# Kernel tuning notes

Hardware: AMD Instinct MI355X
Metric: run time of the kernel (lower is better)

The kernel has to match this reference:

```python
import jax, jax.numpy as jnp
import numpy as np

B, S, D, H = 2, 2048, 1024, 16
HEAD_DIM = D // H
SCALE = HEAD_DIM ** -0.5


def setup_inputs() -> dict:
    key = jax.random.key(0)
    k1, k2, k3 = jax.random.split(key, 3)
    x = jax.random.normal(k1, (B, S, D), dtype=jnp.float32)
    # torch nn.Linear convention: weight is [out_features, in_features], y = x @ W.T + b
    W_qkv = jax.random.normal(k2, (3 * D, D), dtype=jnp.float32) * 0.02  # qkv Linear, bias=False
    W_out = jax.random.normal(k3, (D, D), dtype=jnp.float32) * 0.02
    b_out = jnp.zeros((D,), dtype=jnp.float32)
    return {"x": x, "W_qkv": W_qkv, "W_out": W_out, "b_out": b_out}


def reference(x, W_qkv, W_out, b_out):
    b, s, d_model = x.shape
    # qkv projection (no bias), then split 'b c (qkv h d) -> qkv b h c d'
    qkv = (x @ W_qkv.T).reshape(b, s, 3, H, HEAD_DIM).transpose(2, 0, 3, 1, 4)
    q, k, v = qkv[0], qkv[1], qkv[2]  # each [b, h, s, hd]
    # naive full attention: scores materialized as [b, h, s, s]
    attn = jax.nn.softmax(jnp.einsum('bhxd,bhyd->bhxy', q, k) * SCALE, axis=-1)
    # dropout is identity (rate 0 / eval mode)
    o = jnp.einsum('bhxy,bhyd->bhxd', attn, v)
    o = o.transpose(0, 2, 1, 3).reshape(b, s, d_model)  # 'b h c d -> b c (h d)'
    return o @ W_out.T + b_out
```

## Files before the change

### kernel.cpp

```cpp
#include <hip/hip_runtime.h>


typedef __attribute__((ext_vector_type(8))) short short8;
typedef __attribute__((ext_vector_type(4))) float f32x4;
typedef __attribute__((ext_vector_type(2))) unsigned int uint32x2;
typedef unsigned short ushort_t;
typedef unsigned int uint32;

#define AS1 __attribute__((address_space(1)))
#define AS3 __attribute__((address_space(3)))

__device__ __forceinline__ void gload_lds16(const void* gp, void* lp) {
    __builtin_amdgcn_global_load_lds((const AS1 void*)gp, (AS3 void*)lp, 16, 0, 0);
}

#if __has_builtin(__builtin_amdgcn_exp2f)
#define EXP2F(x) __builtin_amdgcn_exp2f(x)
#else
#define EXP2F(x) exp2f(x)
#endif

__device__ __forceinline__ uint32 rhu(float f) { return __float_as_uint(f) + 0x8000u; }
#if __has_builtin(__builtin_amdgcn_perm)
__device__ __forceinline__ uint32 pk2bf(float a, float b) {
    return __builtin_amdgcn_perm(rhu(b), rhu(a), 0x07060302u);
}
#else
__device__ __forceinline__ uint32 pk2bf(float a, float b) {
    return (rhu(a) >> 16) | (rhu(b) & 0xffff0000u);
}
#endif
__device__ __forceinline__ ushort_t f2bf(float f) { return (ushort_t)(rhu(f) >> 16); }

#if __has_builtin(__builtin_amdgcn_permlane32_swap)
__device__ __forceinline__ void plane32(uint32& a, uint32& b) {
    uint32x2 r = __builtin_amdgcn_permlane32_swap(a, b, false, false);
    a = r[0]; b = r[1];
}
#else
__device__ __forceinline__ void plane32(uint32& a, uint32& b) {
    asm("v_permlane32_swap_b32 %0, %1" : "+v"(a), "+v"(b));
}
#endif
#if __has_builtin(__builtin_amdgcn_permlane16_swap)
__device__ __forceinline__ void plane16(uint32& a, uint32& b) {
    uint32x2 r = __builtin_amdgcn_permlane16_swap(a, b, false, false);
    a = r[0]; b = r[1];
}
#else
__device__ __forceinline__ void plane16(uint32& a, uint32& b) {
    asm("v_permlane16_swap_b32 %0, %1" : "+v"(a), "+v"(b));
}
#endif

__global__ void cvt_all(const float* __restrict__ x, ushort_t* __restrict__ xb,
                        const float* __restrict__ wq, ushort_t* __restrict__ wqb,
                        const float* __restrict__ wo, ushort_t* __restrict__ wob) {
    int blk = blockIdx.x;
    const float* in; ushort_t* out;
    if (blk < 4096)      { in = x;  out = xb;  }
    else if (blk < 7168) { in = wq; out = wqb; blk -= 4096; }
    else                 { in = wo; out = wob; blk -= 7168; }
    const int i = (blk * 256 + threadIdx.x) * 4;
    const float4 v = *(const float4*)(in + i);
    uint2 pk;
    pk.x = pk2bf(v.x, v.y);
    pk.y = pk2bf(v.z, v.w);
    *(uint2*)(out + i) = pk;
}

__global__ __launch_bounds__(512, 2)
void gemm_qkv(const ushort_t* __restrict__ A, const ushort_t* __restrict__ B,
              ushort_t* __restrict__ Cb, ushort_t* __restrict__ vT, float qScale) {
    __shared__ ushort_t smem[4][16384];
    const int K = 1024;
    const int tid = threadIdx.x;
    const int wave = tid >> 6, lane = tid & 63;
    const int quad = lane >> 4, l16 = lane & 15;
    const int wr = wave >> 2, wc = wave & 3;

    int bid = blockIdx.x + 12 * blockIdx.y;
    bid = (bid & 7) * 24 + (bid >> 3);
    const int nBase = (bid % 12) * 256, mBase = (bid / 12) * 256;

    f32x4 acc[8][4];
#pragma unroll
    for (int i = 0; i < 8; i++)
#pragma unroll
        for (int j = 0; j < 4; j++) acc[i][j] = (f32x4){0.f, 0.f, 0.f, 0.f};

    const int ar = tid >> 2;
    const int ac = ((tid & 3) ^ ((ar >> 1) & 3)) * 8;
    const int rsw = (l16 >> 1) & 3;

    const ushort_t* aptr = A + (size_t)(mBase + ar) * K + ac;
    const ushort_t* bptr = B + (size_t)(nBase + ar) * K + ac;

#define G1_STAGE(t)                                                                   \
    {                                                                                 \
        ushort_t* d = &smem[(t) & 3][0];                                              \
        const int k0 = (t) * 32;                                                      \
        gload_lds16(aptr + k0, d + wave * 512);                                       \
        gload_lds16(aptr + (size_t)128 * K + k0, d + 4096 + wave * 512);              \
        gload_lds16(bptr + k0, d + 8192 + wave * 512);                                \
        gload_lds16(bptr + (size_t)128 * K + k0, d + 12288 + wave * 512);             \
    }

#define G1_COMPUTE(t)                                                                 \
    {                                                                                 \
        const ushort_t* lA = &smem[(t) & 3][0];                                       \
        const ushort_t* lB = lA + 8192;                                               \
        short8 af[8], bf[4];                                                          \
        _Pragma("unroll") for (int i = 0; i < 8; i++)                                 \
            af[i] = *(const short8*)(lA + (wr * 128 + i * 16 + l16) * 32 +            \
                                     ((quad ^ rsw) * 8));                             \
        _Pragma("unroll") for (int j = 0; j < 4; j++)                                 \
            bf[j] = *(const short8*)(lB + (wc * 64 + j * 16 + l16) * 32 +             \
                                     ((quad ^ rsw) * 8));                             \
        _Pragma("unroll") for (int i = 0; i < 8; i++)                                 \
            _Pragma("unroll") for (int j = 0; j < 4; j++)                             \
                acc[i][j] = __builtin_amdgcn_mfma_f32_16x16x32_bf16(af[i], bf[j],     \
                                                                    acc[i][j], 0, 0, 0); \
    }

#define G1_SYNC(n)                                                                    \
    asm volatile("s_waitcnt vmcnt(" #n ")" ::: "memory");                             \
    __builtin_amdgcn_s_barrier();                                                     \
    asm volatile("" ::: "memory");

    G1_STAGE(0); G1_STAGE(1); G1_STAGE(2);

#pragma unroll 4
    for (int t = 0; t < 28; ++t) {
        G1_SYNC(8);
        G1_STAGE(t + 3);
        G1_COMPUTE(t);
    }
    { G1_SYNC(8); G1_STAGE(31); G1_COMPUTE(28); }
    { G1_SYNC(8); G1_COMPUTE(29); }
    { G1_SYNC(4); G1_COMPUTE(30); }
    { G1_SYNC(0); G1_COMPUTE(31); }

    if (nBase >= 2048) {
#pragma unroll
        for (int i = 0; i < 8; i++)
#pragma unroll
            for (int j = 0; j < 4; j++) {
                const int row0 = mBase + wr * 128 + i * 16 + quad * 4;
                const int col = nBase + wc * 64 + j * 16 + l16 - 2048;
                const int b = row0 >> 11, s0 = row0 & 2047;
                uint2 pk;
                pk.x = pk2bf(acc[i][j][0], acc[i][j][1]);
                pk.y = pk2bf(acc[i][j][2], acc[i][j][3]);
                *(uint2*)(vT + ((size_t)(b * 16) * 64 + col) * 2048 + s0) = pk;
            }
        return;
    }
    const float cs = (nBase < 1024) ? qScale : 1.0f;
#pragma unroll
    for (int i = 0; i < 8; i++)
#pragma unroll
        for (int j = 0; j < 4; j++)
#pragma unroll
            for (int r = 0; r < 4; r++) {
                const int row = mBase + wr * 128 + i * 16 + quad * 4 + r;
                const int col = nBase + wc * 64 + j * 16 + l16;
                Cb[(size_t)row * 2048 + col] = f2bf(acc[i][j][r] * cs);
            }
}

__global__ __launch_bounds__(256, 2)
void gemm_out(const ushort_t* __restrict__ A, const ushort_t* __restrict__ B,
              float* __restrict__ Cf, const float* __restrict__ bias,
              int M, int N, int K) {
    __shared__ ushort_t lA[2][64 * 64];
    __shared__ ushort_t lB[2][128 * 64];
    const int tid = threadIdx.x;
    const int wave = tid >> 6, lane = tid & 63;
    const int quad = lane >> 4, l16 = lane & 15;
    const int mBase = blockIdx.y * 64, nBase = blockIdx.x * 128;

    f32x4 acc[4][2];
#pragma unroll
    for (int i = 0; i < 4; i++)
#pragma unroll
        for (int j = 0; j < 2; j++) acc[i][j] = (f32x4){0.f, 0.f, 0.f, 0.f};

    const int sr = tid >> 3;
    const int sc = ((tid & 7) ^ (sr & 7)) * 8;
    const int swz = l16 & 7;

    const ushort_t* aptr = A + (size_t)(mBase + sr) * K + sc;
    const ushort_t* bptr = B + (size_t)(nBase + sr) * K + sc;

#define G2_STAGE(buf, k0)                                                              \
    {                                                                                  \
        _Pragma("unroll") for (int c = 0; c < 2; c++)                                  \
            gload_lds16(aptr + (size_t)(c * 32) * K + (k0), lA[buf] + c * 2048 + wave * 512); \
        _Pragma("unroll") for (int c = 0; c < 4; c++)                                  \
            gload_lds16(bptr + (size_t)(c * 32) * K + (k0), lB[buf] + c * 2048 + wave * 512); \
    }

    G2_STAGE(0, 0);
    for (int k0 = 0; k0 < K; k0 += 64) {
        const int cur = (k0 >> 6) & 1;
        __syncthreads();
        if (k0 + 64 < K) G2_STAGE(cur ^ 1, k0 + 64);

#pragma unroll
        for (int ks = 0; ks < 2; ks++) {
            short8 af[4], bf[2];
#pragma unroll
            for (int i = 0; i < 4; i++)
                af[i] = *(const short8*)(lA[cur] + (i * 16 + l16) * 64 + (((ks * 4 + quad) ^ swz) * 8));
#pragma unroll
            for (int j = 0; j < 2; j++)
                bf[j] = *(const short8*)(lB[cur] + (wave * 32 + j * 16 + l16) * 64 + (((ks * 4 + quad) ^ swz) * 8));
#pragma unroll
            for (int i = 0; i < 4; i++)
#pragma unroll
                for (int j = 0; j < 2; j++)
                    acc[i][j] = __builtin_amdgcn_mfma_f32_16x16x32_bf16(af[i], bf[j], acc[i][j], 0, 0, 0);
        }
    }

#pragma unroll
    for (int i = 0; i < 4; i++)
#pragma unroll
        for (int j = 0; j < 2; j++)
#pragma unroll
            for (int r = 0; r < 4; r++) {
                const int row = mBase + i * 16 + quad * 4 + r;
                const int col = nBase + wave * 32 + j * 16 + l16;
                Cf[(size_t)row * N + col] = acc[i][j][r] + bias[col];
            }
}

__global__ __launch_bounds__(512, 4)
void attn_flash(const ushort_t* __restrict__ qk, const ushort_t* __restrict__ vT,
                ushort_t* __restrict__ o) {
    __shared__ ushort_t smem[28672];

    const int tid = threadIdx.x;
    const int wave = tid >> 6, lane = tid & 63;
    const int quad = lane >> 4, l16 = lane & 15;
    const int qg = wave & 3, kg = wave >> 2;
    const int bh = blockIdx.x, b = bh >> 4, h = bh & 15;
    const size_t rowBase = (size_t)b * 2048;
    const int qCol = h * 64, kCol = 1024 + h * 64;
    const int qRow0 = blockIdx.y * 128;
    const int swz = l16 & 7;

    const int sr = tid >> 3;
    const int sc = ((tid & 7) ^ (sr & 7)) * 8;

#pragma unroll
    for (int cc = 0; cc < 2; cc++)
        gload_lds16(qk + (rowBase + qRow0 + cc * 64 + sr) * 2048 + qCol + sc,
                    smem + 20480 + cc * 4096 + wave * 512);
    __syncthreads();
    short8 qf[2][2];
#pragma unroll
    for (int qt = 0; qt < 2; qt++)
#pragma unroll
        for (int ks = 0; ks < 2; ks++)
            qf[qt][ks] = *(const short8*)(smem + 20480 + (qg * 32 + qt * 16 + l16) * 64 +
                                          (((ks * 4 + quad) ^ swz) * 8));

    short8 onesA;
#pragma unroll
    for (int i = 0; i < 8; i++) onesA[i] = (short)0x3F80;

    f32x4 oacc[4][2];
    f32x4 lacc[2];
#pragma unroll
    for (int qt = 0; qt < 2; qt++) {
        lacc[qt] = (f32x4){0.f, 0.f, 0.f, 0.f};
#pragma unroll
        for (int dt = 0; dt < 4; dt++) oacc[dt][qt] = (f32x4){0.f, 0.f, 0.f, 0.f};
    }

    const ushort_t* kptr = qk + (rowBase + sr) * 2048 + kCol + sc;
    const ushort_t* vptr = vT + ((size_t)bh * 64 + sr) * 2048 + sc;

    f32x4 sacc[2][2];
    short8 pfA[2], pfB[2];

#define AT_STAGE(kbi, vbi, kt)                                                         \
    {                                                                                  \
        gload_lds16(kptr + (size_t)((kt) * 64) * 2048, smem + (kbi) * 4096 + wave * 512); \
        gload_lds16(vptr + (kt) * 64, smem + 8192 + (vbi) * 4096 + wave * 512);        \
    }

#define S_BLOCK(cur)                                                                   \
    {                                                                                  \
        const ushort_t* lK = smem + (cur) * 4096;                                      \
        _Pragma("unroll") for (int mh = 0; mh < 2; mh++) {                             \
            const int krow = kg * 32 + mh * 16 + l16;                                  \
            const short8 k0 = *(const short8*)(lK + krow * 64 + ((quad ^ swz) * 8));   \
            const short8 k1 = *(const short8*)(lK + krow * 64 + (((4 + quad) ^ swz) * 8)); \
            __builtin_amdgcn_s_setprio(1);                                             \
            _Pragma("unroll") for (int qt = 0; qt < 2; qt++) {                         \
                f32x4 t = (f32x4){0.f, 0.f, 0.f, 0.f};                                 \
                t = __builtin_amdgcn_mfma_f32_16x16x32_bf16(k0, qf[qt][0], t, 0, 0, 0); \
                t = __builtin_amdgcn_mfma_f32_16x16x32_bf16(k1, qf[qt][1], t, 0, 0, 0); \
                sacc[mh][qt] = t;                                                      \
            }                                                                          \
            __builtin_amdgcn_s_setprio(0);                                             \
        }                                                                              \
    }

#define EXPPK_BLOCK(pfdst)                                                             \
    _Pragma("unroll") for (int qt = 0; qt < 2; qt++) {                                 \
        uint32 a0 = pk2bf(EXP2F(sacc[0][qt][0]), EXP2F(sacc[0][qt][1]));               \
        uint32 a1 = pk2bf(EXP2F(sacc[0][qt][2]), EXP2F(sacc[0][qt][3]));               \
        uint32 b0 = pk2bf(EXP2F(sacc[1][qt][0]), EXP2F(sacc[1][qt][1]));               \
        uint32 b1 = pk2bf(EXP2F(sacc[1][qt][2]), EXP2F(sacc[1][qt][3]));               \
        plane32(a0, b0); plane16(a0, b0);                                              \
        plane32(a1, b1); plane16(a1, b1);                                              \
        union { uint32 u[4]; short8 s; } w_;                                           \
        w_.u[0] = a0; w_.u[1] = a1; w_.u[2] = b0; w_.u[3] = b1;                        \
        pfdst[qt] = w_.s;                                                              \
    }

#define PV_BLOCK(vbi, pf)                                                              \
    {                                                                                  \
        const ushort_t* lV = smem + 8192 + (vbi) * 4096;                               \
        _Pragma("unroll") for (int qt = 0; qt < 2; qt++)                               \
            lacc[qt] = __builtin_amdgcn_mfma_f32_16x16x32_bf16(onesA, pf[qt], lacc[qt], 0, 0, 0); \
        __builtin_amdgcn_s_setprio(1);                                                 \
        _Pragma("unroll") for (int dt = 0; dt < 4; dt++) {                             \
            const short8 vf = *(const short8*)(lV + (dt * 16 + l16) * 64 +             \
                                               (((kg * 4 + quad) ^ swz) * 8));         \
            _Pragma("unroll") for (int qt = 0; qt < 2; qt++)                           \
                oacc[dt][qt] = __builtin_amdgcn_mfma_f32_16x16x32_bf16(vf, pf[qt], oacc[dt][qt], 0, 0, 0); \
        }                                                                              \
        __builtin_amdgcn_s_setprio(0);                                                 \
    }

    AT_STAGE(0, 0, 0);

    __syncthreads();
    AT_STAGE(1, 1, 1);
    S_BLOCK(0);
    EXPPK_BLOCK(pfA);

    int vs = 2, vp = 0;
    for (int kt = 1; kt <= 29; kt += 2) {
        __syncthreads();
        AT_STAGE(0, vs, kt + 1);
        S_BLOCK(1);
        PV_BLOCK(vp, pfA);
        EXPPK_BLOCK(pfB);
        vs = (vs == 2) ? 0 : vs + 1;
        vp = (vp == 2) ? 0 : vp + 1;
        __syncthreads();
        AT_STAGE(1, vs, kt + 2);
        S_BLOCK(0);
        PV_BLOCK(vp, pfB);
        EXPPK_BLOCK(pfA);
        vs = (vs == 2) ? 0 : vs + 1;
        vp = (vp == 2) ? 0 : vp + 1;
    }

    __syncthreads();
    S_BLOCK(1);
    PV_BLOCK(0, pfA);
    EXPPK_BLOCK(pfB);
    PV_BLOCK(1, pfB);

    __syncthreads();
    float* red = (float*)smem;
    if (kg == 1) {
#pragma unroll
        for (int qt = 0; qt < 2; qt++) {
            if (quad == 0) red[8192 + qg * 32 + qt * 16 + l16] = lacc[qt][0];
#pragma unroll
            for (int dt = 0; dt < 4; dt++)
                *(f32x4*)(red + (((qg * 4 + dt) * 2 + qt) * 64 + lane) * 4) = oacc[dt][qt];
        }
    }
    __syncthreads();
    if (kg == 0) {
        float linv[2];
#pragma unroll
        for (int qt = 0; qt < 2; qt++)
            linv[qt] = 1.0f / (lacc[qt][0] + red[8192 + qg * 32 + qt * 16 + l16]);
#pragma unroll
        for (int qt = 0; qt < 2; qt++) {
            const size_t row = rowBase + qRow0 + qg * 32 + qt * 16 + l16;
#pragma unroll
            for (int dt = 0; dt < 4; dt++) {
                const f32x4 r = *(const f32x4*)(red + (((qg * 4 + dt) * 2 + qt) * 64 + lane) * 4);
                uint2 pk;
                pk.x = pk2bf((oacc[dt][qt][0] + r[0]) * linv[qt],
                             (oacc[dt][qt][1] + r[1]) * linv[qt]);
                pk.y = pk2bf((oacc[dt][qt][2] + r[2]) * linv[qt],
                             (oacc[dt][qt][3] + r[3]) * linv[qt]);
                *(uint2*)(o + row * 1024 + h * 64 + dt * 16 + quad * 4) = pk;
            }
        }
    }
}

extern "C" void kernel_launch(void* const* d_in, const int* in_sizes, int n_in,
                              void* d_out, int out_size, void* d_ws, size_t ws_size,
                              hipStream_t stream) {
    const float* x    = (const float*)d_in[0];
    const float* Wqkv = (const float*)d_in[1];
    const float* Wout = (const float*)d_in[2];
    const float* bout = (const float*)d_in[3];
    float* out = (float*)d_out;

    ushort_t* xb    = (ushort_t*)d_ws;
    ushort_t* wqkvb = xb + (size_t)4096 * 1024;
    ushort_t* woutb = wqkvb + (size_t)3072 * 1024;
    ushort_t* qkb   = woutb + (size_t)1024 * 1024;
    ushort_t* vTb   = qkb + (size_t)4096 * 2048;
    ushort_t* ob    = xb;

    const float SC = 0.125f * 1.44269504089f;

    cvt_all<<<8192, 256, 0, stream>>>(x, xb, Wqkv, wqkvb, Wout, woutb);
    gemm_qkv<<<dim3(12, 16), 512, 0, stream>>>(xb, wqkvb, qkb, vTb, SC);
    attn_flash<<<dim3(32, 16), 512, 0, stream>>>(qkb, vTb, ob);
    gemm_out<<<dim3(8, 64), 256, 0, stream>>>(ob, woutb, out, bout, 4096, 1024, 1024);
}
```

Baseline: 170.1 us.

## Fuse fp32-to-bf16 conversion into GEMM loaders and drop separate convert kernel

Removes the standalone cvt_all kernel and has both GEMMs load fp32 x and weights directly, converting to bf16 in registers before writing LDS. The QKV GEMM is retiled from 256x256 blocks with 512 threads and a 4-stage async global-to-LDS pipeline to 128x192 blocks with 256 threads and register double buffering. This saves one launch and a full bf16 round trip through memory. In exchange it reads twice the bytes per load, replaces the async LDS loads with register staging, and weights are reconverted by every block.

```diff
diff --git a/kernel.cpp b/kernel.cpp
--- a/kernel.cpp
+++ b/kernel.cpp
@@ -53,131 +53,125 @@
 }
 #endif
 
-__global__ void cvt_all(const float* __restrict__ x, ushort_t* __restrict__ xb,
-                        const float* __restrict__ wq, ushort_t* __restrict__ wqb,
-                        const float* __restrict__ wo, ushort_t* __restrict__ wob) {
-    int blk = blockIdx.x;
-    const float* in; ushort_t* out;
-    if (blk < 4096)      { in = x;  out = xb;  }
-    else if (blk < 7168) { in = wq; out = wqb; blk -= 4096; }
-    else                 { in = wo; out = wob; blk -= 7168; }
-    const int i = (blk * 256 + threadIdx.x) * 4;
-    const float4 v = *(const float4*)(in + i);
-    uint2 pk;
-    pk.x = pk2bf(v.x, v.y);
-    pk.y = pk2bf(v.z, v.w);
-    *(uint2*)(out + i) = pk;
-}
-
-__global__ __launch_bounds__(512, 2)
-void gemm_qkv(const ushort_t* __restrict__ A, const ushort_t* __restrict__ B,
+__global__ __launch_bounds__(256, 2)
+void gemm_qkv(const float* __restrict__ A, const float* __restrict__ B,
               ushort_t* __restrict__ Cb, ushort_t* __restrict__ vT, float qScale) {
-    __shared__ ushort_t smem[4][16384];
+    __shared__ ushort_t lA[2][128 * 32];
+    __shared__ ushort_t lB[2][192 * 32];
     const int K = 1024;
     const int tid = threadIdx.x;
     const int wave = tid >> 6, lane = tid & 63;
     const int quad = lane >> 4, l16 = lane & 15;
-    const int wr = wave >> 2, wc = wave & 3;
-
-    int bid = blockIdx.x + 12 * blockIdx.y;
-    bid = (bid & 7) * 24 + (bid >> 3);
-    const int nBase = (bid % 12) * 256, mBase = (bid / 12) * 256;
-
-    f32x4 acc[8][4];
+    const int rsw = (l16 >> 1) & 3;
+
+    int bid = blockIdx.x + 16 * blockIdx.y;
+    bid = (bid & 7) * 64 + (bid >> 3);
+    const int nBase = (bid & 15) * 192, mBase = (bid >> 4) * 128;
+
+    f32x4 acc[8][3];
 #pragma unroll
     for (int i = 0; i < 8; i++)
 #pragma unroll
-        for (int j = 0; j < 4; j++) acc[i][j] = (f32x4){0.f, 0.f, 0.f, 0.f};
-
-    const int ar = tid >> 2;
-    const int ac = ((tid & 3) ^ ((ar >> 1) & 3)) * 8;
-    const int rsw = (l16 >> 1) & 3;
-
-    const ushort_t* aptr = A + (size_t)(mBase + ar) * K + ac;
-    const ushort_t* bptr = B + (size_t)(nBase + ar) * K + ac;
-
-#define G1_STAGE(t)                                                                   \
+        for (int j = 0; j < 3; j++) acc[i][j] = (f32x4){0.f, 0.f, 0.f, 0.f};
+
+    const int srow = tid >> 2, slc = tid & 3;
+    const int rs = (srow >> 1) & 3;
+    const int gc = slc ^ rs;
+
+    float4 ra[2][2], rb[3][2];
+
+#define QLOAD(k0)                                                                     \
     {                                                                                 \
-        ushort_t* d = &smem[(t) & 3][0];                                              \
-        const int k0 = (t) * 32;                                                      \
-        gload_lds16(aptr + k0, d + wave * 512);                                       \
-        gload_lds16(aptr + (size_t)128 * K + k0, d + 4096 + wave * 512);              \
-        gload_lds16(bptr + k0, d + 8192 + wave * 512);                                \
-        gload_lds16(bptr + (size_t)128 * K + k0, d + 12288 + wave * 512);             \
-    }
-
-#define G1_COMPUTE(t)                                                                 \
+        _Pragma("unroll") for (int p = 0; p < 2; p++) {                               \
+            const float* s = A + (size_t)(mBase + p * 64 + srow) * K + (k0) + gc * 8; \
+            ra[p][0] = *(const float4*)(s);                                           \
+            ra[p][1] = *(const float4*)(s + 4);                                       \
+        }                                                                             \
+        _Pragma("unroll") for (int p = 0; p < 3; p++) {                               \
+            const float* s = B + (size_t)(nBase + p * 64 + srow) * K + (k0) + gc * 8; \
+            rb[p][0] = *(const float4*)(s);                                           \
+            rb[p][1] = *(const float4*)(s + 4);                                       \
+        }                                                                             \
+    }
+
+#define QCVTW(buf)                                                                    \
     {                                                                                 \
-        const ushort_t* lA = &smem[(t) & 3][0];                                       \
-        const ushort_t* lB = lA + 8192;                                               \
-        short8 af[8], bf[4];                                                          \
+        _Pragma("unroll") for (int p = 0; p < 2; p++) {                               \
+            uint4 w;                                                                  \
+            w.x = pk2bf(ra[p][0].x, ra[p][0].y); w.y = pk2bf(ra[p][0].z, ra[p][0].w); \
+            w.z = pk2bf(ra[p][1].x, ra[p][1].y); w.w = pk2bf(ra[p][1].z, ra[p][1].w); \
+            *(uint4*)(&lA[buf][(p * 64 + srow) * 32 + slc * 8]) = w;                  \
+        }                                                                             \
+        _Pragma("unroll") for (int p = 0; p < 3; p++) {                               \
+            uint4 w;                                                                  \
+            w.x = pk2bf(rb[p][0].x, rb[p][0].y); w.y = pk2bf(rb[p][0].z, rb[p][0].w); \
+            w.z = pk2bf(rb[p][1].x, rb[p][1].y); w.w = pk2bf(rb[p][1].z, rb[p][1].w); \
+            *(uint4*)(&lB[buf][(p * 64 + srow) * 32 + slc * 8]) = w;                  \
+        }                                                                             \
+    }
+
+#define QCOMP(buf)                                                                    \
+    {                                                                                 \
+        short8 af[8], bf[3];                                                          \
         _Pragma("unroll") for (int i = 0; i < 8; i++)                                 \
-            af[i] = *(const short8*)(lA + (wr * 128 + i * 16 + l16) * 32 +            \
-                                     ((quad ^ rsw) * 8));                             \
-        _Pragma("unroll") for (int j = 0; j < 4; j++)                                 \
-            bf[j] = *(const short8*)(lB + (wc * 64 + j * 16 + l16) * 32 +             \
-                                     ((quad ^ rsw) * 8));                             \
+            af[i] = *(const short8*)(&lA[buf][(i * 16 + l16) * 32 + ((quad ^ rsw) * 8)]); \
+        _Pragma("unroll") for (int j = 0; j < 3; j++)                                 \
+            bf[j] = *(const short8*)(&lB[buf][(wave * 48 + j * 16 + l16) * 32 +       \
+                                              ((quad ^ rsw) * 8)]);                   \
         _Pragma("unroll") for (int i = 0; i < 8; i++)                                 \
-            _Pragma("unroll") for (int j = 0; j < 4; j++)                             \
+            _Pragma("unroll") for (int j = 0; j < 3; j++)                             \
                 acc[i][j] = __builtin_amdgcn_mfma_f32_16x16x32_bf16(af[i], bf[j],     \
                                                                     acc[i][j], 0, 0, 0); \
     }
 
-#define G1_SYNC(n)                                                                    \
-    asm volatile("s_waitcnt vmcnt(" #n ")" ::: "memory");                             \
-    __builtin_amdgcn_s_barrier();                                                     \
-    asm volatile("" ::: "memory");
-
-    G1_STAGE(0); G1_STAGE(1); G1_STAGE(2);
-
-#pragma unroll 4
-    for (int t = 0; t < 28; ++t) {
-        G1_SYNC(8);
-        G1_STAGE(t + 3);
-        G1_COMPUTE(t);
-    }
-    { G1_SYNC(8); G1_STAGE(31); G1_COMPUTE(28); }
-    { G1_SYNC(8); G1_COMPUTE(29); }
-    { G1_SYNC(4); G1_COMPUTE(30); }
-    { G1_SYNC(0); G1_COMPUTE(31); }
-
-    if (nBase >= 2048) {
-#pragma unroll
-        for (int i = 0; i < 8; i++)
-#pragma unroll
-            for (int j = 0; j < 4; j++) {
-                const int row0 = mBase + wr * 128 + i * 16 + quad * 4;
-                const int col = nBase + wc * 64 + j * 16 + l16 - 2048;
+    QLOAD(0);
+    QCVTW(0);
+    QLOAD(32);
+    __syncthreads();
+
+    for (int t = 0; t < 32; ++t) {
+        const int buf = t & 1;
+        QCOMP(buf);
+        if (t < 31) {
+            QCVTW(buf ^ 1);
+            if (t < 30) QLOAD((t + 2) * 32);
+        }
+        __syncthreads();
+    }
+
+#pragma unroll
+    for (int i = 0; i < 8; i++)
+#pragma unroll
+        for (int j = 0; j < 3; j++) {
+            const int colBase = nBase + wave * 48 + j * 16;
+            const int row0 = mBase + i * 16 + quad * 4;
+            if (colBase >= 2048) {
+                const int col = colBase + l16 - 2048;
                 const int b = row0 >> 11, s0 = row0 & 2047;
                 uint2 pk;
                 pk.x = pk2bf(acc[i][j][0], acc[i][j][1]);
                 pk.y = pk2bf(acc[i][j][2], acc[i][j][3]);
                 *(uint2*)(vT + ((size_t)(b * 16) * 64 + col) * 2048 + s0) = pk;
+            } else {
+                const float cs = (colBase < 1024) ? qScale : 1.0f;
+                const int col = colBase + l16;
+#pragma unroll
+                for (int r = 0; r < 4; r++)
+                    Cb[(size_t)(row0 + r) * 2048 + col] = f2bf(acc[i][j][r] * cs);
             }
-        return;
-    }
-    const float cs = (nBase < 1024) ? qScale : 1.0f;
-#pragma unroll
-    for (int i = 0; i < 8; i++)
-#pragma unroll
-        for (int j = 0; j < 4; j++)
-#pragma unroll
-            for (int r = 0; r < 4; r++) {
-                const int row = mBase + wr * 128 + i * 16 + quad * 4 + r;
-                const int col = nBase + wc * 64 + j * 16 + l16;
-                Cb[(size_t)row * 2048 + col] = f2bf(acc[i][j][r] * cs);
-            }
+        }
 }
 
 __global__ __launch_bounds__(256, 2)
-void gemm_out(const ushort_t* __restrict__ A, const ushort_t* __restrict__ B,
-              float* __restrict__ Cf, const float* __restrict__ bias,
-              int M, int N, int K) {
+void gemm_out(const ushort_t* __restrict__ A, const float* __restrict__ B,
+              float* __restrict__ Cf, const float* __restrict__ bias) {
+    const int K = 1024, N = 1024;
     __shared__ ushort_t lA[2][64 * 64];
     __shared__ ushort_t lB[2][128 * 64];
     const int tid = threadIdx.x;
     const int wave = tid >> 6, lane = tid & 63;
     const int quad = lane >> 4, l16 = lane & 15;
+    const int swz = l16 & 7;
     const int mBase = blockIdx.y * 64, nBase = blockIdx.x * 128;
 
     f32x4 acc[4][2];
@@ -186,42 +180,64 @@
 #pragma unroll
         for (int j = 0; j < 2; j++) acc[i][j] = (f32x4){0.f, 0.f, 0.f, 0.f};
 
-    const int sr = tid >> 3;
-    const int sc = ((tid & 7) ^ (sr & 7)) * 8;
-    const int swz = l16 & 7;
-
-    const ushort_t* aptr = A + (size_t)(mBase + sr) * K + sc;
-    const ushort_t* bptr = B + (size_t)(nBase + sr) * K + sc;
-
-#define G2_STAGE(buf, k0)                                                              \
-    {                                                                                  \
-        _Pragma("unroll") for (int c = 0; c < 2; c++)                                  \
-            gload_lds16(aptr + (size_t)(c * 32) * K + (k0), lA[buf] + c * 2048 + wave * 512); \
-        _Pragma("unroll") for (int c = 0; c < 4; c++)                                  \
-            gload_lds16(bptr + (size_t)(c * 32) * K + (k0), lB[buf] + c * 2048 + wave * 512); \
-    }
-
-    G2_STAGE(0, 0);
-    for (int k0 = 0; k0 < K; k0 += 64) {
-        const int cur = (k0 >> 6) & 1;
+    const int srow = tid >> 3, slc = tid & 7;
+    const int gc = slc ^ (srow & 7);
+
+    short8 ra2[2];
+    float4 rb[4][2];
+
+#define OLOAD(k0)                                                                     \
+    {                                                                                 \
+        _Pragma("unroll") for (int c = 0; c < 2; c++)                                 \
+            ra2[c] = *(const short8*)(A + (size_t)(mBase + c * 32 + srow) * K +       \
+                                      (k0) + gc * 8);                                 \
+        _Pragma("unroll") for (int p = 0; p < 4; p++) {                               \
+            const float* s = B + (size_t)(nBase + p * 32 + srow) * K + (k0) + gc * 8; \
+            rb[p][0] = *(const float4*)(s);                                           \
+            rb[p][1] = *(const float4*)(s + 4);                                       \
+        }                                                                             \
+    }
+
+#define OCVTW(buf)                                                                    \
+    {                                                                                 \
+        _Pragma("unroll") for (int c = 0; c < 2; c++)                                 \
+            *(short8*)(&lA[buf][(c * 32 + srow) * 64 + slc * 8]) = ra2[c];            \
+        _Pragma("unroll") for (int p = 0; p < 4; p++) {                               \
+            uint4 w;                                                                  \
+            w.x = pk2bf(rb[p][0].x, rb[p][0].y); w.y = pk2bf(rb[p][0].z, rb[p][0].w); \
+            w.z = pk2bf(rb[p][1].x, rb[p][1].y); w.w = pk2bf(rb[p][1].z, rb[p][1].w); \
+            *(uint4*)(&lB[buf][(p * 32 + srow) * 64 + slc * 8]) = w;                  \
+        }                                                                             \
+    }
+
+#define OCOMP(buf)                                                                    \
+    _Pragma("unroll") for (int ks = 0; ks < 2; ks++) {                                \
+        short8 af[4], bf[2];                                                          \
+        _Pragma("unroll") for (int i = 0; i < 4; i++)                                 \
+            af[i] = *(const short8*)(&lA[buf][(i * 16 + l16) * 64 +                   \
+                                              (((ks * 4 + quad) ^ swz) * 8)]);        \
+        _Pragma("unroll") for (int j = 0; j < 2; j++)                                 \
+            bf[j] = *(const short8*)(&lB[buf][(wave * 32 + j * 16 + l16) * 64 +       \
+                                              (((ks * 4 + quad) ^ swz) * 8)]);        \
+        _Pragma("unroll") for (int i = 0; i < 4; i++)                                 \
+            _Pragma("unroll") for (int j = 0; j < 2; j++)                             \
+                acc[i][j] = __builtin_amdgcn_mfma_f32_16x16x32_bf16(af[i], bf[j],     \
+                                                                    acc[i][j], 0, 0, 0); \
+    }
+
+    OLOAD(0);
+    OCVTW(0);
+    OLOAD(64);
+    __syncthreads();
+
+    for (int t = 0; t < 16; ++t) {
+        const int buf = t & 1;
+        OCOMP(buf);
+        if (t < 15) {
+            OCVTW(buf ^ 1);
+            if (t < 14) OLOAD((t + 2) * 64);
+        }
         __syncthreads();
-        if (k0 + 64 < K) G2_STAGE(cur ^ 1, k0 + 64);
-
-#pragma unroll
-        for (int ks = 0; ks < 2; ks++) {
-            short8 af[4], bf[2];
-#pragma unroll
-            for (int i = 0; i < 4; i++)
-                af[i] = *(const short8*)(lA[cur] + (i * 16 + l16) * 64 + (((ks * 4 + quad) ^ swz) * 8));
-#pragma unroll
-            for (int j = 0; j < 2; j++)
-                bf[j] = *(const short8*)(lB[cur] + (wave * 32 + j * 16 + l16) * 64 + (((ks * 4 + quad) ^ swz) * 8));
-#pragma unroll
-            for (int i = 0; i < 4; i++)
-#pragma unroll
-                for (int j = 0; j < 2; j++)
-                    acc[i][j] = __builtin_amdgcn_mfma_f32_16x16x32_bf16(af[i], bf[j], acc[i][j], 0, 0, 0);
-        }
     }
 
 #pragma unroll
@@ -412,17 +428,13 @@
     const float* bout = (const float*)d_in[3];
     float* out = (float*)d_out;
 
-    ushort_t* xb    = (ushort_t*)d_ws;
-    ushort_t* wqkvb = xb + (size_t)4096 * 1024;
-    ushort_t* woutb = wqkvb + (size_t)3072 * 1024;
-    ushort_t* qkb   = woutb + (size_t)1024 * 1024;
-    ushort_t* vTb   = qkb + (size_t)4096 * 2048;
-    ushort_t* ob    = xb;
+    ushort_t* qkb = (ushort_t*)d_ws;
+    ushort_t* vTb = qkb + (size_t)4096 * 2048;
+    ushort_t* ob  = vTb + (size_t)32 * 64 * 2048;
 
     const float SC = 0.125f * 1.44269504089f;
 
-    cvt_all<<<8192, 256, 0, stream>>>(x, xb, Wqkv, wqkvb, Wout, woutb);
-    gemm_qkv<<<dim3(12, 16), 512, 0, stream>>>(xb, wqkvb, qkb, vTb, SC);
+    gemm_qkv<<<dim3(16, 32), 256, 0, stream>>>(x, Wqkv, qkb, vTb, SC);
     attn_flash<<<dim3(32, 16), 512, 0, stream>>>(qkb, vTb, ob);
-    gemm_out<<<dim3(8, 64), 256, 0, stream>>>(ob, woutb, out, bout, 4096, 1024, 1024);
-}
+    gemm_out<<<dim3(8, 64), 256, 0, stream>>>(ob, Wout, out, bout);
+}
```

Result: no change. 170.8 us (+0.4%).

## Retile QKV GEMM to 128x192 blocks and pipeline output GEMM with 4-stage async loads

Applied to the files above, without the earlier changes.

The QKV projection GEMM moves from 256x256 tiles with 512 threads to 128x192 tiles with 256 threads. That raises the grid from 192 to 512 blocks so the GPU's compute units are better filled, and block IDs are swizzled for L2 locality. The epilogue now picks the vT or Q/K store path per 16-column fragment, because a tile can span both regions. The output GEMM is rewritten to use the same 4-stage global_load_lds pipeline with K=32 steps, explicit vmcnt waits, a swizzled block order and hardcoded dimensions. Smaller tiles reduce data reuse per block, and the mixed-path epilogue adds branching.

```diff
diff --git a/kernel.cpp b/kernel.cpp
--- a/kernel.cpp
+++ b/kernel.cpp
@@ -69,116 +69,113 @@
     *(uint2*)(out + i) = pk;
 }
 
-__global__ __launch_bounds__(512, 2)
+__global__ __launch_bounds__(256, 2)
 void gemm_qkv(const ushort_t* __restrict__ A, const ushort_t* __restrict__ B,
               ushort_t* __restrict__ Cb, ushort_t* __restrict__ vT, float qScale) {
-    __shared__ ushort_t smem[4][16384];
+    __shared__ ushort_t smem[4][10240];
     const int K = 1024;
     const int tid = threadIdx.x;
     const int wave = tid >> 6, lane = tid & 63;
     const int quad = lane >> 4, l16 = lane & 15;
-    const int wr = wave >> 2, wc = wave & 3;
-
-    int bid = blockIdx.x + 12 * blockIdx.y;
-    bid = (bid & 7) * 24 + (bid >> 3);
-    const int nBase = (bid % 12) * 256, mBase = (bid / 12) * 256;
-
-    f32x4 acc[8][4];
+    const int rsw = (l16 >> 1) & 3;
+
+    int bid = blockIdx.x + 16 * blockIdx.y;
+    bid = (bid & 7) * 64 + (bid >> 3);
+    const int nBase = (bid & 15) * 192, mBase = (bid >> 4) * 128;
+
+    f32x4 acc[8][3];
 #pragma unroll
     for (int i = 0; i < 8; i++)
 #pragma unroll
-        for (int j = 0; j < 4; j++) acc[i][j] = (f32x4){0.f, 0.f, 0.f, 0.f};
+        for (int j = 0; j < 3; j++) acc[i][j] = (f32x4){0.f, 0.f, 0.f, 0.f};
 
     const int ar = tid >> 2;
     const int ac = ((tid & 3) ^ ((ar >> 1) & 3)) * 8;
-    const int rsw = (l16 >> 1) & 3;
 
     const ushort_t* aptr = A + (size_t)(mBase + ar) * K + ac;
     const ushort_t* bptr = B + (size_t)(nBase + ar) * K + ac;
 
-#define G1_STAGE(t)                                                                   \
-    {                                                                                 \
-        ushort_t* d = &smem[(t) & 3][0];                                              \
-        const int k0 = (t) * 32;                                                      \
-        gload_lds16(aptr + k0, d + wave * 512);                                       \
-        gload_lds16(aptr + (size_t)128 * K + k0, d + 4096 + wave * 512);              \
-        gload_lds16(bptr + k0, d + 8192 + wave * 512);                                \
-        gload_lds16(bptr + (size_t)128 * K + k0, d + 12288 + wave * 512);             \
-    }
-
-#define G1_COMPUTE(t)                                                                 \
-    {                                                                                 \
-        const ushort_t* lA = &smem[(t) & 3][0];                                       \
-        const ushort_t* lB = lA + 8192;                                               \
-        short8 af[8], bf[4];                                                          \
-        _Pragma("unroll") for (int i = 0; i < 8; i++)                                 \
-            af[i] = *(const short8*)(lA + (wr * 128 + i * 16 + l16) * 32 +            \
-                                     ((quad ^ rsw) * 8));                             \
-        _Pragma("unroll") for (int j = 0; j < 4; j++)                                 \
-            bf[j] = *(const short8*)(lB + (wc * 64 + j * 16 + l16) * 32 +             \
-                                     ((quad ^ rsw) * 8));                             \
-        _Pragma("unroll") for (int i = 0; i < 8; i++)                                 \
-            _Pragma("unroll") for (int j = 0; j < 4; j++)                             \
-                acc[i][j] = __builtin_amdgcn_mfma_f32_16x16x32_bf16(af[i], bf[j],     \
+#define Q_STAGE(t)                                                                   \
+    {                                                                                \
+        ushort_t* d = &smem[(t) & 3][0];                                             \
+        const int k0 = (t) * 32;                                                     \
+        gload_lds16(aptr + k0, d + wave * 512);                                      \
+        gload_lds16(aptr + (size_t)64 * K + k0, d + 2048 + wave * 512);              \
+        gload_lds16(bptr + k0, d + 4096 + wave * 512);                               \
+        gload_lds16(bptr + (size_t)64 * K + k0, d + 6144 + wave * 512);              \
+        gload_lds16(bptr + (size_t)128 * K + k0, d + 8192 + wave * 512);             \
+    }
+
+#define Q_COMP(t)                                                                    \
+    {                                                                                \
+        const ushort_t* lA = &smem[(t) & 3][0];                                      \
+        const ushort_t* lB = lA + 4096;                                              \
+        short8 af[8], bf[3];                                                         \
+        _Pragma("unroll") for (int i = 0; i < 8; i++)                                \
+            af[i] = *(const short8*)(lA + (i * 16 + l16) * 32 + ((quad ^ rsw) * 8)); \
+        _Pragma("unroll") for (int j = 0; j < 3; j++)                                \
+            bf[j] = *(const short8*)(lB + (wave * 48 + j * 16 + l16) * 32 +          \
+                                     ((quad ^ rsw) * 8));                            \
+        _Pragma("unroll") for (int i = 0; i < 8; i++)                                \
+            _Pragma("unroll") for (int j = 0; j < 3; j++)                            \
+                acc[i][j] = __builtin_amdgcn_mfma_f32_16x16x32_bf16(af[i], bf[j],    \
                                                                     acc[i][j], 0, 0, 0); \
     }
 
-#define G1_SYNC(n)                                                                    \
-    asm volatile("s_waitcnt vmcnt(" #n ")" ::: "memory");                             \
-    __builtin_amdgcn_s_barrier();                                                     \
+#define Q_SYNC(n)                                                                    \
+    asm volatile("s_waitcnt vmcnt(" #n ")" ::: "memory");                            \
+    __builtin_amdgcn_s_barrier();                                                    \
     asm volatile("" ::: "memory");
 
-    G1_STAGE(0); G1_STAGE(1); G1_STAGE(2);
+    Q_STAGE(0); Q_STAGE(1); Q_STAGE(2);
 
 #pragma unroll 4
     for (int t = 0; t < 28; ++t) {
-        G1_SYNC(8);
-        G1_STAGE(t + 3);
-        G1_COMPUTE(t);
-    }
-    { G1_SYNC(8); G1_STAGE(31); G1_COMPUTE(28); }
-    { G1_SYNC(8); G1_COMPUTE(29); }
-    { G1_SYNC(4); G1_COMPUTE(30); }
-    { G1_SYNC(0); G1_COMPUTE(31); }
-
-    if (nBase >= 2048) {
-#pragma unroll
-        for (int i = 0; i < 8; i++)
-#pragma unroll
-            for (int j = 0; j < 4; j++) {
-                const int row0 = mBase + wr * 128 + i * 16 + quad * 4;
-                const int col = nBase + wc * 64 + j * 16 + l16 - 2048;
+        Q_SYNC(10);
+        Q_STAGE(t + 3);
+        Q_COMP(t);
+    }
+    { Q_SYNC(10); Q_STAGE(31); Q_COMP(28); }
+    { Q_SYNC(10); Q_COMP(29); }
+    { Q_SYNC(5);  Q_COMP(30); }
+    { Q_SYNC(0);  Q_COMP(31); }
+
+#pragma unroll
+    for (int i = 0; i < 8; i++)
+#pragma unroll
+        for (int j = 0; j < 3; j++) {
+            const int colBase = nBase + wave * 48 + j * 16;
+            const int row0 = mBase + i * 16 + quad * 4;
+            if (colBase >= 2048) {
+                const int col = colBase + l16 - 2048;
                 const int b = row0 >> 11, s0 = row0 & 2047;
                 uint2 pk;
                 pk.x = pk2bf(acc[i][j][0], acc[i][j][1]);
                 pk.y = pk2bf(acc[i][j][2], acc[i][j][3]);
                 *(uint2*)(vT + ((size_t)(b * 16) * 64 + col) * 2048 + s0) = pk;
+            } else {
+                const float cs = (colBase < 1024) ? qScale : 1.0f;
+                const int col = colBase + l16;
+#pragma unroll
+                for (int r = 0; r < 4; r++)
+                    Cb[(size_t)(row0 + r) * 2048 + col] = f2bf(acc[i][j][r] * cs);
             }
-        return;
-    }
-    const float cs = (nBase < 1024) ? qScale : 1.0f;
-#pragma unroll
-    for (int i = 0; i < 8; i++)
-#pragma unroll
-        for (int j = 0; j < 4; j++)
-#pragma unroll
-            for (int r = 0; r < 4; r++) {
-                const int row = mBase + wr * 128 + i * 16 + quad * 4 + r;
-                const int col = nBase + wc * 64 + j * 16 + l16;
-                Cb[(size_t)row * 2048 + col] = f2bf(acc[i][j][r] * cs);
-            }
+        }
 }
 
 __global__ __launch_bounds__(256, 2)
 void gemm_out(const ushort_t* __restrict__ A, const ushort_t* __restrict__ B,
-              float* __restrict__ Cf, const float* __restrict__ bias,
-              int M, int N, int K) {
-    __shared__ ushort_t lA[2][64 * 64];
-    __shared__ ushort_t lB[2][128 * 64];
+              float* __restrict__ Cf, const float* __restrict__ bias) {
+    __shared__ ushort_t smem[4][6144];
+    const int K = 1024, N = 1024;
     const int tid = threadIdx.x;
     const int wave = tid >> 6, lane = tid & 63;
     const int quad = lane >> 4, l16 = lane & 15;
-    const int mBase = blockIdx.y * 64, nBase = blockIdx.x * 128;
+    const int rsw = (l16 >> 1) & 3;
+
+    int bid = blockIdx.x + 8 * blockIdx.y;
+    bid = (bid & 7) * 64 + (bid >> 3);
+    const int nBase = (bid & 7) * 128, mBase = (bid >> 3) * 64;
 
     f32x4 acc[4][2];
 #pragma unroll
@@ -186,43 +183,49 @@
 #pragma unroll
         for (int j = 0; j < 2; j++) acc[i][j] = (f32x4){0.f, 0.f, 0.f, 0.f};
 
-    const int sr = tid >> 3;
-    const int sc = ((tid & 7) ^ (sr & 7)) * 8;
-    const int swz = l16 & 7;
-
-    const ushort_t* aptr = A + (size_t)(mBase + sr) * K + sc;
-    const ushort_t* bptr = B + (size_t)(nBase + sr) * K + sc;
-
-#define G2_STAGE(buf, k0)                                                              \
-    {                                                                                  \
-        _Pragma("unroll") for (int c = 0; c < 2; c++)                                  \
-            gload_lds16(aptr + (size_t)(c * 32) * K + (k0), lA[buf] + c * 2048 + wave * 512); \
-        _Pragma("unroll") for (int c = 0; c < 4; c++)                                  \
-            gload_lds16(bptr + (size_t)(c * 32) * K + (k0), lB[buf] + c * 2048 + wave * 512); \
-    }
-
-    G2_STAGE(0, 0);
-    for (int k0 = 0; k0 < K; k0 += 64) {
-        const int cur = (k0 >> 6) & 1;
-        __syncthreads();
-        if (k0 + 64 < K) G2_STAGE(cur ^ 1, k0 + 64);
-
-#pragma unroll
-        for (int ks = 0; ks < 2; ks++) {
-            short8 af[4], bf[2];
-#pragma unroll
-            for (int i = 0; i < 4; i++)
-                af[i] = *(const short8*)(lA[cur] + (i * 16 + l16) * 64 + (((ks * 4 + quad) ^ swz) * 8));
-#pragma unroll
-            for (int j = 0; j < 2; j++)
-                bf[j] = *(const short8*)(lB[cur] + (wave * 32 + j * 16 + l16) * 64 + (((ks * 4 + quad) ^ swz) * 8));
-#pragma unroll
-            for (int i = 0; i < 4; i++)
-#pragma unroll
-                for (int j = 0; j < 2; j++)
-                    acc[i][j] = __builtin_amdgcn_mfma_f32_16x16x32_bf16(af[i], bf[j], acc[i][j], 0, 0, 0);
-        }
-    }
+    const int ar = tid >> 2;
+    const int ac = ((tid & 3) ^ ((ar >> 1) & 3)) * 8;
+
+    const ushort_t* aptr = A + (size_t)(mBase + ar) * K + ac;
+    const ushort_t* bptr = B + (size_t)(nBase + ar) * K + ac;
+
+#define O_STAGE(t)                                                                   \
+    {                                                                                \
+        ushort_t* d = &smem[(t) & 3][0];                                             \
+        const int k0 = (t) * 32;                                                     \
+        gload_lds16(aptr + k0, d + wave * 512);                                      \
+        gload_lds16(bptr + k0, d + 2048 + wave * 512);                               \
+        gload_lds16(bptr + (size_t)64 * K + k0, d + 4096 + wave * 512);              \
+    }
+
+#define O_COMP(t)                                                                    \
+    {                                                                                \
+        const ushort_t* lA = &smem[(t) & 3][0];                                      \
+        const ushort_t* lB = lA + 2048;                                              \
+        short8 af[4], bf[2];                                                         \
+        _Pragma("unroll") for (int i = 0; i < 4; i++)                                \
+            af[i] = *(const short8*)(lA + (i * 16 + l16) * 32 + ((quad ^ rsw) * 8)); \
+        _Pragma("unroll") for (int j = 0; j < 2; j++)                                \
+            bf[j] = *(const short8*)(lB + (wave * 32 + j * 16 + l16) * 32 +          \
+                                     ((quad ^ rsw) * 8));                            \
+        _Pragma("unroll") for (int i = 0; i < 4; i++)                                \
+            _Pragma("unroll") for (int j = 0; j < 2; j++)                            \
+                acc[i][j] = __builtin_amdgcn_mfma_f32_16x16x32_bf16(af[i], bf[j],    \
+                                                                    acc[i][j], 0, 0, 0); \
+    }
+
+    O_STAGE(0); O_STAGE(1); O_STAGE(2);
+
+#pragma unroll 4
+    for (int t = 0; t < 28; ++t) {
+        Q_SYNC(6);
+        O_STAGE(t + 3);
+        O_COMP(t);
+    }
+    { Q_SYNC(6); O_STAGE(31); O_COMP(28); }
+    { Q_SYNC(6); O_COMP(29); }
+    { Q_SYNC(3); O_COMP(30); }
+    { Q_SYNC(0); O_COMP(31); }
 
 #pragma unroll
     for (int i = 0; i < 4; i++)
@@ -422,7 +425,7 @@
     const float SC = 0.125f * 1.44269504089f;
 
     cvt_all<<<8192, 256, 0, stream>>>(x, xb, Wqkv, wqkvb, Wout, woutb);
-    gemm_qkv<<<dim3(12, 16), 512, 0, stream>>>(xb, wqkvb, qkb, vTb, SC);
+    gemm_qkv<<<dim3(16, 32), 256, 0, stream>>>(xb, wqkvb, qkb, vTb, SC);
     attn_flash<<<dim3(32, 16), 512, 0, stream>>>(qkb, vTb, ob);
-    gemm_out<<<dim3(8, 64), 256, 0, stream>>>(ob, woutb, out, bout, 4096, 1024, 1024);
-}
+    gemm_out<<<dim3(8, 64), 256, 0, stream>>>(ob, woutb, out, bout);
+}
```

After: 171.1 us. Within noise of the previous version (+0.6%).
